# Performance work log

Measured on AMD Instinct MI355X. Metric: run time of the kernel, lower is better.

Reference implementation:

```python
import jax, jax.numpy as jnp
import numpy as np

H = 1024
V = 50257
S = 4096

def setup_inputs() -> dict:
    key = jax.random.key(0)
    ks = jax.random.split(key, 16)
    s = 0.02
    return {
        "word_input": jax.random.randint(ks[0], (1,), 0, V),
        "h0": jax.random.normal(ks[1], (1, 1, H), jnp.float32),
        "c0": jax.random.normal(ks[2], (1, 1, H), jnp.float32),
        "encoder_outputs": jax.random.normal(ks[3], (S, 1, H), jnp.float32),
        "embedding": jax.random.normal(ks[4], (V, H), jnp.float32) * s,
        "W_ih": jax.random.normal(ks[5], (4 * H, H), jnp.float32) * s,
        "W_hh": jax.random.normal(ks[6], (4 * H, H), jnp.float32) * s,
        "b_ih": jnp.zeros((4 * H,), jnp.float32),
        "b_hh": jnp.zeros((4 * H,), jnp.float32),
        "attn_W": jax.random.normal(ks[7], (H, H), jnp.float32) * s,
        "attn_b": jnp.zeros((H,), jnp.float32),
        "out_W": jax.random.normal(ks[8], (V, 2 * H), jnp.float32) * s,
        "out_b": jnp.zeros((V,), jnp.float32),
    }


def reference(word_input, h0, c0, encoder_outputs, embedding, W_ih, W_hh,
              b_ih, b_hh, attn_W, attn_b, out_W, out_b):
    # Embedding lookup: (1, H)
    x = embedding[word_input]
    h_prev = h0[0]  # (1, H)
    c_prev = c0[0]  # (1, H)
    # Single-step single-layer LSTM (PyTorch gate order i, f, g, o)
    gates = x @ W_ih.T + b_ih + h_prev @ W_hh.T + b_hh  # (1, 4H)
    i_g, f_g, g_g, o_g = jnp.split(gates, 4, axis=1)
    c_new = jax.nn.sigmoid(f_g) * c_prev + jax.nn.sigmoid(i_g) * jnp.tanh(g_g)
    h_new = jax.nn.sigmoid(o_g) * jnp.tanh(c_new)  # (1, H) == rnn_output
    # Attention ('general'): score_i = hidden . (W_a e_i + b_a), vectorized over S
    enc = encoder_outputs[:, 0, :]  # (S, H)
    scores = (enc @ attn_W.T + attn_b) @ h_new[0]  # (S,)
    attn_w = jax.nn.softmax(scores)  # (S,)
    context = attn_w @ enc  # (H,)
    # Output projection + log_softmax
    feat = jnp.concatenate([h_new[0], context])  # (2H,)
    logits = feat @ out_W.T + out_b  # (V,)
    output = jax.nn.log_softmax(logits)[None, :]  # (1, V)
    return (output, h_new[None], c_new[None], attn_w[None, None, :])
```

## Files before the change

kernel.cpp:

```cpp
#include <hip/hip_runtime.h>
#include <math.h>

#define H 1024
#define V 50257
#define S 4096

#define OUT_H (V)
#define OUT_C (V + H)
#define OUT_A (V + 2 * H)

#define WS_LOGITS 0
#define WS_V      50260
#define WS_CTX    (WS_V + H)
#define WS_SCORES (WS_CTX + H)
#define WS_SB     (WS_SCORES + S)
#define WS_PM     (WS_SB + 4)
#define WS_PL     (WS_PM + 32)
#define WS_H      (WS_PL + 32)

#define GEMV_A_BLOCKS 938
#define GEMV_S_BLOCKS 938
#define GEMV_C_BLOCKS 1266
#define GEMV_S_BASE 15008
#define GEMV_C_BASE 30016

__device__ __forceinline__ float wave_red(float v) {
#pragma unroll
    for (int off = 32; off > 0; off >>= 1) v += __shfl_xor(v, off, 64);
    return v;
}

__device__ __forceinline__ void gemv_h_block(
    const float* __restrict__ outW, const float* __restrict__ outb,
    const float* __restrict__ h, float* __restrict__ ws, int base, int t)
{
    int wave = t >> 6, lane = t & 63;
    const float4* h4 = (const float4*)h;
    float4 hv0 = h4[lane], hv1 = h4[lane + 64], hv2 = h4[lane + 128], hv3 = h4[lane + 192];
    int r0 = base + wave * 4;
#pragma unroll
    for (int i = 0; i < 4; i++) {
        int r = r0 + i;
        if (r < V) {
            const float4* w4 = (const float4*)(outW + (size_t)r * 2048);
            float4 a = w4[lane];
            float acc = a.x * hv0.x + a.y * hv0.y + a.z * hv0.z + a.w * hv0.w;
            a = w4[lane + 64];  acc += a.x * hv1.x + a.y * hv1.y + a.z * hv1.z + a.w * hv1.w;
            a = w4[lane + 128]; acc += a.x * hv2.x + a.y * hv2.y + a.z * hv2.z + a.w * hv2.w;
            a = w4[lane + 192]; acc += a.x * hv3.x + a.y * hv3.y + a.z * hv3.z + a.w * hv3.w;
            acc = wave_red(acc);
            if (lane == 0) ws[WS_LOGITS + r] = acc + outb[r];
        }
    }
}

__global__ __launch_bounds__(256) void lstm_kernel(
    const int* __restrict__ word, const float* __restrict__ emb,
    const float* __restrict__ Wih, const float* __restrict__ Whh,
    const float* __restrict__ bih, const float* __restrict__ bhh,
    const float* __restrict__ h0, const float* __restrict__ c0,
    float* __restrict__ out, float* __restrict__ ws)
{
    int b = blockIdx.x, t = threadIdx.x;
    if (b >= H) {
        int z = b - H;
        if (z < 4)      ws[WS_V + z * 256 + t] = 0.f;
        else if (z < 8) ws[WS_CTX + (z - 4) * 256 + t] = 0.f;
        else if (t == 0) ws[WS_SB] = 0.f;
        return;
    }
    int wave = t >> 6, lane = t & 63;
    int row = b + wave * H;
    const float4* x4 = (const float4*)(emb + (size_t)word[0] * H);
    const float4* h4 = (const float4*)h0;
    const float4* wi = (const float4*)(Wih + (size_t)row * H);
    const float4* wh = (const float4*)(Whh + (size_t)row * H);
    float acc = 0.f;
#pragma unroll
    for (int k = 0; k < 4; k++) {
        int idx = lane + 64 * k;
        float4 a = wi[idx], xb = x4[idx];
        acc += a.x * xb.x + a.y * xb.y + a.z * xb.z + a.w * xb.w;
        float4 c = wh[idx], hb = h4[idx];
        acc += c.x * hb.x + c.y * hb.y + c.z * hb.z + c.w * hb.w;
    }
    acc = wave_red(acc);
    __shared__ float gates[4];
    if (lane == 0) gates[wave] = acc;
    __syncthreads();
    if (t == 0) {
        int j = b;
        float ig = gates[0] + bih[j]         + bhh[j];
        float fg = gates[1] + bih[j + H]     + bhh[j + H];
        float gg = gates[2] + bih[j + 2 * H] + bhh[j + 2 * H];
        float og = gates[3] + bih[j + 3 * H] + bhh[j + 3 * H];
        float si = 1.f / (1.f + expf(-ig));
        float sf = 1.f / (1.f + expf(-fg));
        float so = 1.f / (1.f + expf(-og));
        float cn = sf * c0[j] + si * tanhf(gg);
        float hn = so * tanhf(cn);
        out[OUT_C + j] = cn;
        out[OUT_H + j] = hn;
        ws[WS_H + j]   = hn;
    }
}

__global__ __launch_bounds__(256) void attnv_kernel(
    const float* __restrict__ attn_W, const float* __restrict__ attn_b,
    const float* __restrict__ out, const float* __restrict__ outW,
    const float* __restrict__ outb, float* ws)
{
    int b = blockIdx.x, t = threadIdx.x;
    if (b < 128) {
        int jb = b & 31, kb = b >> 5;
        __shared__ float hs[32];
        if (t < 32) hs[t] = out[OUT_H + jb * 32 + t];
        __syncthreads();
        float acc = 0.f;
        const float* base = attn_W + (size_t)(jb * 32) * H + kb * 256 + t;
#pragma unroll 8
        for (int jj = 0; jj < 32; jj++) acc += hs[jj] * base[(size_t)jj * H];
        atomicAdd(&ws[WS_V + kb * 256 + t], acc);
        if (kb == 0 && t < 32) {
            float p = hs[t] * attn_b[jb * 32 + t];
#pragma unroll
            for (int off = 16; off > 0; off >>= 1) p += __shfl_xor(p, off, 32);
            if (t == 0) atomicAdd(&ws[WS_SB], p);
        }
    } else {
        gemv_h_block(outW, outb, ws + WS_H, ws, (b - 128) * 16, t);
    }
}

__global__ __launch_bounds__(256) void scores_kernel(
    const float* __restrict__ enc, const float* __restrict__ outW,
    const float* __restrict__ outb, float* ws)
{
    int b = blockIdx.x, t = threadIdx.x;
    int wave = t >> 6, lane = t & 63;
    if (b < S / 4) {
        int s = b * 4 + wave;
        const float4* e4 = (const float4*)(enc + (size_t)s * H);
        const float4* v4 = (const float4*)(ws + WS_V);
        float acc = 0.f;
#pragma unroll
        for (int it = 0; it < 4; it++) {
            float4 a = e4[lane + 64 * it];
            float4 bb = v4[lane + 64 * it];
            acc += a.x * bb.x + a.y * bb.y + a.z * bb.z + a.w * bb.w;
        }
        acc = wave_red(acc);
        if (lane == 0) ws[WS_SCORES + s] = acc + ws[WS_SB];
    } else {
        gemv_h_block(outW, outb, ws + WS_H, ws, GEMV_S_BASE + (b - S / 4) * 16, t);
    }
}

__global__ __launch_bounds__(1024) void softmax_kernel(
    const float* __restrict__ ws, float* __restrict__ out)
{
    int t = threadIdx.x;
    float x[4];
    float m = -INFINITY;
#pragma unroll
    for (int i = 0; i < 4; i++) { x[i] = ws[WS_SCORES + t + i * 1024]; m = fmaxf(m, x[i]); }
    __shared__ float red[1024];
    __shared__ float sm, sl;
    red[t] = m; __syncthreads();
    for (int off = 512; off > 0; off >>= 1) { if (t < off) red[t] = fmaxf(red[t], red[t + off]); __syncthreads(); }
    if (t == 0) sm = red[0];
    __syncthreads();
    m = sm;
    float l = 0.f;
#pragma unroll
    for (int i = 0; i < 4; i++) { x[i] = expf(x[i] - m); l += x[i]; }
    red[t] = l; __syncthreads();
    for (int off = 512; off > 0; off >>= 1) { if (t < off) red[t] += red[t + off]; __syncthreads(); }
    if (t == 0) sl = red[0];
    __syncthreads();
    float inv = 1.f / sl;
#pragma unroll
    for (int i = 0; i < 4; i++) out[OUT_A + t + i * 1024] = x[i] * inv;
}

__global__ __launch_bounds__(256) void context_kernel(
    const float* __restrict__ enc, const float* __restrict__ out,
    const float* __restrict__ outW, const float* __restrict__ outb, float* ws)
{
    int b = blockIdx.x, t = threadIdx.x;
    if (b < 256) {
        int sb = b >> 2, kb = b & 3;
        const float* aw = out + OUT_A;
        float acc = 0.f;
        for (int ss = 0; ss < 64; ss++) {
            int s = sb * 64 + ss;
            acc += aw[s] * enc[(size_t)s * H + kb * 256 + t];
        }
        atomicAdd(&ws[WS_CTX + kb * 256 + t], acc);
    } else {
        gemv_h_block(outW, outb, ws + WS_H, ws, GEMV_C_BASE + (b - 256) * 16, t);
    }
}

__global__ __launch_bounds__(256) void logits_ctx_kernel(
    const float* __restrict__ outW, float* ws)
{
    int t = threadIdx.x;
    int wave = t >> 6, lane = t & 63;
    const float4* c4 = (const float4*)(ws + WS_CTX);
    float4 cv0 = c4[lane], cv1 = c4[lane + 64], cv2 = c4[lane + 128], cv3 = c4[lane + 192];
    int r0 = blockIdx.x * 16 + wave * 4;
#pragma unroll
    for (int i = 0; i < 4; i++) {
        int r = r0 + i;
        if (r < V) {
            const float4* w4 = (const float4*)(outW + (size_t)r * 2048 + 1024);
            float4 a = w4[lane];
            float acc = a.x * cv0.x + a.y * cv0.y + a.z * cv0.z + a.w * cv0.w;
            a = w4[lane + 64];  acc += a.x * cv1.x + a.y * cv1.y + a.z * cv1.z + a.w * cv1.w;
            a = w4[lane + 128]; acc += a.x * cv2.x + a.y * cv2.y + a.z * cv2.z + a.w * cv2.w;
            a = w4[lane + 192]; acc += a.x * cv3.x + a.y * cv3.y + a.z * cv3.z + a.w * cv3.w;
            acc = wave_red(acc);
            if (lane == 0) ws[WS_LOGITS + r] += acc;
        }
    }
}

__global__ __launch_bounds__(256) void lse_partial_kernel(float* ws)
{
    int t = threadIdx.x, b = blockIdx.x;
    float m = -INFINITY, l = 0.f;
    for (int i = b * 256 + t; i < V; i += 32 * 256) {
        float x = ws[WS_LOGITS + i];
        float nm = fmaxf(m, x);
        l = l * expf(m - nm) + expf(x - nm);
        m = nm;
    }
    __shared__ float sm[256], sl[256];
    sm[t] = m; sl[t] = l; __syncthreads();
    for (int off = 128; off > 0; off >>= 1) {
        if (t < off) {
            float m2 = sm[t + off], l2 = sl[t + off];
            float nm = fmaxf(sm[t], m2);
            sl[t] = sl[t] * expf(sm[t] - nm) + l2 * expf(m2 - nm);
            sm[t] = nm;
        }
        __syncthreads();
    }
    if (t == 0) { ws[WS_PM + b] = sm[0]; ws[WS_PL + b] = sl[0]; }
}

__global__ __launch_bounds__(256) void lsout_kernel(const float* __restrict__ ws, float* __restrict__ out)
{
    __shared__ float fm, fl;
    int t = threadIdx.x;
    if (t == 0) {
        float m = -INFINITY, l = 0.f;
        for (int p = 0; p < 32; p++) {
            float m2 = ws[WS_PM + p], l2 = ws[WS_PL + p];
            float nm = fmaxf(m, m2);
            l = l * expf(m - nm) + l2 * expf(m2 - nm);
            m = nm;
        }
        fm = m; fl = logf(l);
    }
    __syncthreads();
    int i = blockIdx.x * 256 + t;
    if (i < V) out[i] = ws[WS_LOGITS + i] - fm - fl;
}

extern "C" void kernel_launch(void* const* d_in, const int* in_sizes, int n_in,
                              void* d_out, int out_size, void* d_ws, size_t ws_size,
                              hipStream_t stream) {
    const int*   word   = (const int*)d_in[0];
    const float* h0     = (const float*)d_in[1];
    const float* c0     = (const float*)d_in[2];
    const float* enc    = (const float*)d_in[3];
    const float* emb    = (const float*)d_in[4];
    const float* Wih    = (const float*)d_in[5];
    const float* Whh    = (const float*)d_in[6];
    const float* bih    = (const float*)d_in[7];
    const float* bhh    = (const float*)d_in[8];
    const float* attn_W = (const float*)d_in[9];
    const float* attn_b = (const float*)d_in[10];
    const float* outW   = (const float*)d_in[11];
    const float* outb   = (const float*)d_in[12];
    float* out = (float*)d_out;
    float* ws  = (float*)d_ws;

    lstm_kernel<<<H + 9, 256, 0, stream>>>(word, emb, Wih, Whh, bih, bhh, h0, c0, out, ws);
    attnv_kernel<<<128 + GEMV_A_BLOCKS, 256, 0, stream>>>(attn_W, attn_b, out, outW, outb, ws);
    scores_kernel<<<S / 4 + GEMV_S_BLOCKS, 256, 0, stream>>>(enc, outW, outb, ws);
    softmax_kernel<<<1, 1024, 0, stream>>>(ws, out);
    context_kernel<<<256 + GEMV_C_BLOCKS, 256, 0, stream>>>(enc, out, outW, outb, ws);
    logits_ctx_kernel<<<(V + 15) / 16, 256, 0, stream>>>(outW, ws);
    lse_partial_kernel<<<32, 256, 0, stream>>>(ws);
    lsout_kernel<<<(V + 255) / 256, 256, 0, stream>>>(ws, out);
}
```

Baseline: 675.5 us.

## Fuse LSE partials into context logits kernel and fill softmax launch with GEMV work

The separate log-sum-exp partial kernel is removed. Each logits_ctx block now keeps an online max/sum over its 16 finished logits and writes one partial. lsout then has every block reduce all 3142 partials in parallel, instead of one thread folding 32. The single-block softmax launch now also carries 96 extra 1024-thread blocks of the hidden-half output GEMV, with the other GEMV block counts rebalanced, so the GPU is not idle during the serial softmax. This saves one launch and a re-read of the logits, at the cost of redundant partial reductions in every lsout block.

```diff
diff --git a/kernel.cpp b/kernel.cpp
--- a/kernel.cpp
+++ b/kernel.cpp
@@ -15,14 +15,18 @@
 #define WS_SCORES (WS_CTX + H)
 #define WS_SB     (WS_SCORES + S)
 #define WS_PM     (WS_SB + 4)
-#define WS_PL     (WS_PM + 32)
-#define WS_H      (WS_PL + 32)
-
-#define GEMV_A_BLOCKS 938
-#define GEMV_S_BLOCKS 938
-#define GEMV_C_BLOCKS 1266
-#define GEMV_S_BASE 15008
-#define GEMV_C_BASE 30016
+#define WS_PL     (WS_PM + 3144)
+#define WS_H      (WS_PL + 3144)
+
+#define LCB 3142
+
+#define GEMV_A_BLOCKS 900
+#define GEMV_S_BLOCKS 900
+#define GEMV_SM_BLOCKS 96
+#define GEMV_C_BLOCKS 958
+#define GEMV_S_BASE  14400
+#define GEMV_SM_BASE 28800
+#define GEMV_C_BASE  34944
 
 __device__ __forceinline__ float wave_red(float v) {
 #pragma unroll
@@ -157,13 +161,18 @@
 }
 
 __global__ __launch_bounds__(1024) void softmax_kernel(
-    const float* __restrict__ ws, float* __restrict__ out)
+    const float* __restrict__ ws_c, float* __restrict__ out,
+    const float* __restrict__ outW, const float* __restrict__ outb, float* ws)
 {
     int t = threadIdx.x;
+    if (blockIdx.x > 0) {
+        gemv_h_block(outW, outb, ws + WS_H, ws, GEMV_SM_BASE + (blockIdx.x - 1) * 64, t);
+        return;
+    }
     float x[4];
     float m = -INFINITY;
 #pragma unroll
-    for (int i = 0; i < 4; i++) { x[i] = ws[WS_SCORES + t + i * 1024]; m = fmaxf(m, x[i]); }
+    for (int i = 0; i < 4; i++) { x[i] = ws_c[WS_SCORES + t + i * 1024]; m = fmaxf(m, x[i]); }
     __shared__ float red[1024];
     __shared__ float sm, sl;
     red[t] = m; __syncthreads();
@@ -210,6 +219,7 @@
     const float4* c4 = (const float4*)(ws + WS_CTX);
     float4 cv0 = c4[lane], cv1 = c4[lane + 64], cv2 = c4[lane + 128], cv3 = c4[lane + 192];
     int r0 = blockIdx.x * 16 + wave * 4;
+    float pm = -INFINITY, pl = 0.f;
 #pragma unroll
     for (int i = 0; i < 4; i++) {
         int r = r0 + i;
@@ -221,22 +231,46 @@
             a = w4[lane + 128]; acc += a.x * cv2.x + a.y * cv2.y + a.z * cv2.z + a.w * cv2.w;
             a = w4[lane + 192]; acc += a.x * cv3.x + a.y * cv3.y + a.z * cv3.z + a.w * cv3.w;
             acc = wave_red(acc);
-            if (lane == 0) ws[WS_LOGITS + r] += acc;
-        }
-    }
-}
-
-__global__ __launch_bounds__(256) void lse_partial_kernel(float* ws)
-{
-    int t = threadIdx.x, b = blockIdx.x;
+            if (lane == 0) {
+                float fin = ws[WS_LOGITS + r] + acc;
+                ws[WS_LOGITS + r] = fin;
+                float nm = fmaxf(pm, fin);
+                pl = pl * expf(pm - nm) + expf(fin - nm);
+                pm = nm;
+            }
+        }
+    }
+    __shared__ float sm4[4], sl4[4];
+    if (lane == 0) { sm4[wave] = pm; sl4[wave] = pl; }
+    __syncthreads();
+    if (t == 0) {
+        float m = sm4[0], l = sl4[0];
+#pragma unroll
+        for (int w = 1; w < 4; w++) {
+            float m2 = sm4[w], l2 = sl4[w];
+            float nm = fmaxf(m, m2);
+            if (nm > -INFINITY) {
+                l = l * expf(m - nm) + l2 * expf(m2 - nm);
+                m = nm;
+            }
+        }
+        ws[WS_PM + blockIdx.x] = m;
+        ws[WS_PL + blockIdx.x] = l;
+    }
+}
+
+__global__ __launch_bounds__(256) void lsout_kernel(const float* __restrict__ ws, float* __restrict__ out)
+{
+    int t = threadIdx.x;
     float m = -INFINITY, l = 0.f;
-    for (int i = b * 256 + t; i < V; i += 32 * 256) {
-        float x = ws[WS_LOGITS + i];
-        float nm = fmaxf(m, x);
-        l = l * expf(m - nm) + expf(x - nm);
+    for (int i = t; i < LCB; i += 256) {
+        float m2 = ws[WS_PM + i], l2 = ws[WS_PL + i];
+        float nm = fmaxf(m, m2);
+        l = l * expf(m - nm) + l2 * expf(m2 - nm);
         m = nm;
     }
     __shared__ float sm[256], sl[256];
+    __shared__ float fm, fl;
     sm[t] = m; sl[t] = l; __syncthreads();
     for (int off = 128; off > 0; off >>= 1) {
         if (t < off) {
@@ -247,23 +281,7 @@
         }
         __syncthreads();
     }
-    if (t == 0) { ws[WS_PM + b] = sm[0]; ws[WS_PL + b] = sl[0]; }
-}
-
-__global__ __launch_bounds__(256) void lsout_kernel(const float* __restrict__ ws, float* __restrict__ out)
-{
-    __shared__ float fm, fl;
-    int t = threadIdx.x;
-    if (t == 0) {
-        float m = -INFINITY, l = 0.f;
-        for (int p = 0; p < 32; p++) {
-            float m2 = ws[WS_PM + p], l2 = ws[WS_PL + p];
-            float nm = fmaxf(m, m2);
-            l = l * expf(m - nm) + l2 * expf(m2 - nm);
-            m = nm;
-        }
-        fm = m; fl = logf(l);
-    }
+    if (t == 0) { fm = sm[0]; fl = logf(sl[0]); }
     __syncthreads();
     int i = blockIdx.x * 256 + t;
     if (i < V) out[i] = ws[WS_LOGITS + i] - fm - fl;
@@ -291,9 +309,8 @@
     lstm_kernel<<<H + 9, 256, 0, stream>>>(word, emb, Wih, Whh, bih, bhh, h0, c0, out, ws);
     attnv_kernel<<<128 + GEMV_A_BLOCKS, 256, 0, stream>>>(attn_W, attn_b, out, outW, outb, ws);
     scores_kernel<<<S / 4 + GEMV_S_BLOCKS, 256, 0, stream>>>(enc, outW, outb, ws);
-    softmax_kernel<<<1, 1024, 0, stream>>>(ws, out);
+    softmax_kernel<<<1 + GEMV_SM_BLOCKS, 1024, 0, stream>>>(ws, out, outW, outb, ws);
     context_kernel<<<256 + GEMV_C_BLOCKS, 256, 0, stream>>>(enc, out, outW, outb, ws);
-    logits_ctx_kernel<<<(V + 15) / 16, 256, 0, stream>>>(outW, ws);
-    lse_partial_kernel<<<32, 256, 0, stream>>>(ws);
+    logits_ctx_kernel<<<LCB, 256, 0, stream>>>(outW, ws);
     lsout_kernel<<<(V + 255) / 256, 256, 0, stream>>>(ws, out);
 }
```

Result: no change. 670.6 us (-0.7%).
